# Optimization experiments

Measured on AMD Instinct MI355X. Metric: run time of the kernel, lower is better.

The kernel has to match this reference:

```python
import jax, jax.numpy as jnp
import numpy as np

N_HEADS = 8
N_POINTS = 4


def _bilinear_sample(vl, g, Hl, Wl):
    # vl: [B, nH, Hl*Wl, hd] level values; g: [B, Q, nH, P, 2] sampling locs in [0,1] (x, y)
    # Emulates torch grid_sample(mode='bilinear', padding_mode='zeros', align_corners=False)
    B, Q, nH, P, _ = g.shape
    hd = vl.shape[-1]
    x = g[..., 0] * Wl - 0.5
    y = g[..., 1] * Hl - 0.5
    x0f = jnp.floor(x)
    y0f = jnp.floor(y)
    x0 = x0f.astype(jnp.int32)
    y0 = y0f.astype(jnp.int32)
    wx1 = x - x0f
    wy1 = y - y0f

    def corner(xi, yi, w):
        valid = (xi >= 0) & (xi < Wl) & (yi >= 0) & (yi < Hl)
        idx = jnp.clip(yi, 0, Hl - 1) * Wl + jnp.clip(xi, 0, Wl - 1)  # [B,Q,nH,P]
        idx = idx.transpose(0, 2, 1, 3).reshape(B, nH, Q * P)
        gathered = jnp.take_along_axis(vl, idx[..., None], axis=2)  # [B,nH,Q*P,hd]
        wm = (w * valid.astype(w.dtype)).transpose(0, 2, 1, 3).reshape(B, nH, Q * P)
        return gathered * wm[..., None]

    s = (corner(x0, y0, (1.0 - wx1) * (1.0 - wy1))
         + corner(x0 + 1, y0, wx1 * (1.0 - wy1))
         + corner(x0, y0 + 1, (1.0 - wx1) * wy1)
         + corner(x0 + 1, y0 + 1, wx1 * wy1))
    return s.reshape(B, nH, Q, P, hd)


def setup_inputs() -> dict:
    key = jax.random.key(0)
    ks = jax.random.split(key, 12)
    B, Q, D = 32, 300, 256
    L, P, nH = 4, N_POINTS, N_HEADS
    shapes = np.array([[80, 80], [40, 40], [20, 20], [10, 10]], dtype=np.int32)
    V = int((shapes[:, 0] * shapes[:, 1]).sum())  # 8500
    lsi = np.concatenate([[0], np.cumsum(shapes[:, 0] * shapes[:, 1])[:-1]]).astype(np.int32)
    sd = 1.0 / np.sqrt(D)
    return {
        'query': jax.random.normal(ks[0], (B, Q, D), jnp.float32),
        'reference_points': jax.random.uniform(ks[1], (B, Q, L, 2), jnp.float32),
        'value': jax.random.normal(ks[2], (B, V, D), jnp.float32),
        'spatial_shapes': jnp.asarray(shapes),
        'level_start_index': jnp.asarray(lsi),
        'W_off': jax.random.normal(ks[3], (D, nH * L * P * 2), jnp.float32) * sd,
        'b_off': jax.random.normal(ks[4], (nH * L * P * 2,), jnp.float32) * 0.5,
        'W_attn': jax.random.normal(ks[5], (D, nH * L * P), jnp.float32) * sd,
        'b_attn': jax.random.normal(ks[6], (nH * L * P,), jnp.float32) * 0.1,
        'W_val': jax.random.normal(ks[7], (D, D), jnp.float32) * sd,
        'b_val': jnp.zeros((D,), jnp.float32),
        'W_out': jax.random.normal(ks[8], (D, D), jnp.float32) * sd,
        'b_out': jnp.zeros((D,), jnp.float32),
    }


def reference(query, reference_points, value, spatial_shapes, level_start_index,
              W_off, b_off, W_attn, b_attn, W_val, b_val, W_out, b_out):
    shapes = np.asarray(spatial_shapes)  # static level shapes
    B, Q, D = query.shape
    nH, P = N_HEADS, N_POINTS
    L = shapes.shape[0]
    hd = D // nH

    val = value @ W_val + b_val  # [B,V,D]
    val = val.reshape(B, -1, nH, hd).transpose(0, 2, 1, 3)  # [B,nH,V,hd]

    off = (query @ W_off + b_off).reshape(B, Q, nH, L, P, 2)
    attn = jax.nn.softmax((query @ W_attn + b_attn).reshape(B, Q, nH, L * P), axis=-1)
    attn = attn.reshape(B, Q, nH, L, P)

    # normalizer is (W_l, H_l)
    norm = jnp.asarray(np.stack([shapes[:, 1], shapes[:, 0]], -1), jnp.float32)  # [L,2]
    loc = reference_points[:, :, None, :, None, :] + off / norm[None, None, None, :, None, :]

    out = jnp.zeros((B, Q, nH, hd), query.dtype)
    start = 0
    for lvl in range(L):
        Hl, Wl = int(shapes[lvl, 0]), int(shapes[lvl, 1])
        vl = val[:, :, start:start + Hl * Wl, :]  # [B,nH,HW,hd]
        sampled = _bilinear_sample(vl, loc[:, :, :, lvl], Hl, Wl)  # [B,nH,Q,P,hd]
        out = out + jnp.einsum('bnqpd,bqnp->bqnd', sampled, attn[:, :, :, lvl])
        start += Hl * Wl

    return out.reshape(B, Q, D) @ W_out + b_out
```

## Files before the change

### kernel.cpp

```cpp
#include <hip/hip_runtime.h>
#include <math.h>
#include <stdint.h>

#define NB 32
#define NQ 300
#define ND 256
#define NH 8
#define HD 32
#define NL 4
#define NP 4
#define V_TOT 8500
#define BQ_TOT (NB*NQ)
#define MVAL (NB*V_TOT)
#define NOA 384

typedef short v8s __attribute__((ext_vector_type(8)));
typedef float v4f __attribute__((ext_vector_type(4)));

#define AS1 __attribute__((address_space(1)))
#define AS3 __attribute__((address_space(3)))

__device__ __forceinline__ void copy16_async(const void* g, void* l) {
#if __has_builtin(__builtin_amdgcn_global_load_lds)
    __builtin_amdgcn_global_load_lds((const AS1 unsigned int*)g,
                                     (AS3 unsigned int*)l, 16, 0, 0);
#else
    *(uint4*)l = *(const uint4*)g;
#endif
}

__device__ __forceinline__ unsigned short f2bf_rne(float x) {
    unsigned u = __float_as_uint(x);
    u += 0x7fffu + ((u >> 16) & 1u);
    return (unsigned short)(u >> 16);
}
__device__ __forceinline__ float bf2f(unsigned short b) {
    return __uint_as_float(((unsigned)b) << 16);
}

__device__ __forceinline__ int swz_pos(int n, int k) {
    const int base = k & ~31;
    const int o = (k >> 3) & 3;
    const int op = o ^ ((n >> 1) & 3);
    return n * 256 + base + (op << 3) + (k & 7);
}

__global__ __launch_bounds__(256) void prep_weights(
    const float* __restrict__ W_val, const float* __restrict__ W_off,
    const float* __restrict__ W_attn, const float* __restrict__ W_out,
    const float* __restrict__ b_off, const float* __restrict__ b_attn,
    unsigned short* __restrict__ Bval_h, unsigned short* __restrict__ Bval_l,
    unsigned short* __restrict__ Boa_h,  unsigned short* __restrict__ Boa_l,
    unsigned short* __restrict__ Bout_h, unsigned short* __restrict__ Bout_l,
    float* __restrict__ b_oa)
{
    const int t = blockIdx.x * 256 + threadIdx.x;
    if (t < 65536) {
        const int n = t >> 8, k = t & 255;
        const float x = W_val[k * 256 + n];
        const unsigned short hi = f2bf_rne(x);
        const unsigned short lo = f2bf_rne(x - bf2f(hi));
        const int p = swz_pos(n, k);
        Bval_h[p] = hi; Bval_l[p] = lo;
    } else if (t < 65536 + 98304) {
        const int t2 = t - 65536;
        const int n = t2 >> 8, k = t2 & 255;
        const float x = (n < 256) ? W_off[k * 256 + n] : W_attn[k * 128 + (n - 256)];
        const unsigned short hi = f2bf_rne(x);
        const unsigned short lo = f2bf_rne(x - bf2f(hi));
        const int p = swz_pos(n, k);
        Boa_h[p] = hi; Boa_l[p] = lo;
    } else if (t < 229376) {
        const int t3 = t - 163840;
        const int n = t3 >> 8, k = t3 & 255;
        const float x = W_out[k * 256 + n];
        const unsigned short hi = f2bf_rne(x);
        const unsigned short lo = f2bf_rne(x - bf2f(hi));
        const int p = swz_pos(n, k);
        Bout_h[p] = hi; Bout_l[p] = lo;
    } else {
        const int t4 = t - 229376;
        if (t4 < NOA) b_oa[t4] = (t4 < 256) ? b_off[t4] : b_attn[t4 - 256];
    }
}

__global__ __launch_bounds__(256) void gemm_a32(
    const float* __restrict__ A,
    const unsigned short* __restrict__ Bh,
    const unsigned short* __restrict__ Bl,
    const float* __restrict__ bias,
    float* __restrict__ Cf,
    unsigned short* __restrict__ Cb,
    int ldc, int mode)
{
    __shared__ unsigned short Ah[2][128][40];
    __shared__ unsigned short Al[2][128][40];
    __shared__ unsigned short Bs[2][2][128][32];

    const int tid  = threadIdx.x;
    const int row0 = blockIdx.x * 128;
    const int col0 = blockIdx.y * 128;
    const int wave = tid >> 6;
    const int lane = tid & 63;
    const int wm   = (wave >> 1) * 64;
    const int wn   = (wave & 1) * 64;
    const int m16  = lane & 15;
    const int quad = lane >> 4;

    int rr[2], oo[2];
#pragma unroll
    for (int i = 0; i < 2; ++i) {
        const int idx = tid + i * 256;
        rr[i] = idx >> 2;
        oo[i] = (idx & 3) << 3;
    }

    v4f acc[4][4] = {};
    float fe[2][8];

#pragma unroll
    for (int c = 0; c < 2; ++c) {
        const int linear = (wave * 2 + c) * 1024 + lane * 16;
        const int n   = linear >> 6;
        const int off = linear & 63;
        copy16_async((const char*)Bh + ((size_t)(col0 + n) * 256 + 0) * 2 + off,
                     (char*)&Bs[0][0][0][0] + linear);
        copy16_async((const char*)Bl + ((size_t)(col0 + n) * 256 + 0) * 2 + off,
                     (char*)&Bs[0][1][0][0] + linear);
    }
#pragma unroll
    for (int i = 0; i < 2; ++i) {
        const float4 f0 = *(const float4*)(A + (size_t)(row0 + rr[i]) * 256 + oo[i]);
        const float4 f1 = *(const float4*)(A + (size_t)(row0 + rr[i]) * 256 + oo[i] + 4);
        fe[i][0] = f0.x; fe[i][1] = f0.y; fe[i][2] = f0.z; fe[i][3] = f0.w;
        fe[i][4] = f1.x; fe[i][5] = f1.y; fe[i][6] = f1.z; fe[i][7] = f1.w;
    }
#pragma unroll
    for (int i = 0; i < 2; ++i) {
        unsigned hpk[4], lpk[4];
#pragma unroll
        for (int e = 0; e < 4; ++e) {
            const unsigned u0 = __float_as_uint(fe[i][2*e]);
            const unsigned u1 = __float_as_uint(fe[i][2*e+1]);
            hpk[e] = (u0 >> 16) | (u1 & 0xffff0000u);
            const float l0 = fe[i][2*e]   - __uint_as_float(u0 & 0xffff0000u);
            const float l1 = fe[i][2*e+1] - __uint_as_float(u1 & 0xffff0000u);
            lpk[e] = (__float_as_uint(l0) >> 16) | (__float_as_uint(l1) & 0xffff0000u);
        }
        *(uint4*)&Ah[0][rr[i]][oo[i]] = make_uint4(hpk[0], hpk[1], hpk[2], hpk[3]);
        *(uint4*)&Al[0][rr[i]][oo[i]] = make_uint4(lpk[0], lpk[1], lpk[2], lpk[3]);
    }

    __syncthreads();

    for (int t = 0; t < 8; ++t) {
        const int buf = t & 1;
        const int nb  = buf ^ 1;
        const int k1  = (t + 1) << 5;

        if (t < 7) {
#pragma unroll
            for (int i = 0; i < 2; ++i) {
                const float4 f0 = *(const float4*)(A + (size_t)(row0 + rr[i]) * 256 + k1 + oo[i]);
                const float4 f1 = *(const float4*)(A + (size_t)(row0 + rr[i]) * 256 + k1 + oo[i] + 4);
                fe[i][0] = f0.x; fe[i][1] = f0.y; fe[i][2] = f0.z; fe[i][3] = f0.w;
                fe[i][4] = f1.x; fe[i][5] = f1.y; fe[i][6] = f1.z; fe[i][7] = f1.w;
            }
#pragma unroll
            for (int c = 0; c < 2; ++c) {
                const int linear = (wave * 2 + c) * 1024 + lane * 16;
                const int n   = linear >> 6;
                const int off = linear & 63;
                copy16_async((const char*)Bh + ((size_t)(col0 + n) * 256 + k1) * 2 + off,
                             (char*)&Bs[nb][0][0][0] + linear);
                copy16_async((const char*)Bl + ((size_t)(col0 + n) * 256 + k1) * 2 + off,
                             (char*)&Bs[nb][1][0][0] + linear);
            }
        }

        v8s ah[4], al[4], bh[4], bl[4];
#pragma unroll
        for (int i = 0; i < 4; ++i) {
            ah[i] = *(v8s*)&Ah[buf][wm + i * 16 + m16][quad * 8];
            al[i] = *(v8s*)&Al[buf][wm + i * 16 + m16][quad * 8];
            const int n  = wn + i * 16 + m16;
            const int ko = (quad ^ ((n >> 1) & 3)) << 3;
            bh[i] = *(v8s*)&Bs[buf][0][n][ko];
            bl[i] = *(v8s*)&Bs[buf][1][n][ko];
        }

#pragma unroll
        for (int i = 0; i < 4; ++i)
#pragma unroll
            for (int j = 0; j < 4; ++j) {
                acc[i][j] = __builtin_amdgcn_mfma_f32_16x16x32_bf16(ah[i], bh[j], acc[i][j], 0, 0, 0);
                acc[i][j] = __builtin_amdgcn_mfma_f32_16x16x32_bf16(ah[i], bl[j], acc[i][j], 0, 0, 0);
                acc[i][j] = __builtin_amdgcn_mfma_f32_16x16x32_bf16(al[i], bh[j], acc[i][j], 0, 0, 0);
            }

        if (t < 7) {
#pragma unroll
            for (int i = 0; i < 2; ++i) {
                unsigned hpk[4], lpk[4];
#pragma unroll
                for (int e = 0; e < 4; ++e) {
                    const unsigned u0 = __float_as_uint(fe[i][2*e]);
                    const unsigned u1 = __float_as_uint(fe[i][2*e+1]);
                    hpk[e] = (u0 >> 16) | (u1 & 0xffff0000u);
                    const float l0 = fe[i][2*e]   - __uint_as_float(u0 & 0xffff0000u);
                    const float l1 = fe[i][2*e+1] - __uint_as_float(u1 & 0xffff0000u);
                    lpk[e] = (__float_as_uint(l0) >> 16) | (__float_as_uint(l1) & 0xffff0000u);
                }
                *(uint4*)&Ah[nb][rr[i]][oo[i]] = make_uint4(hpk[0], hpk[1], hpk[2], hpk[3]);
                *(uint4*)&Al[nb][rr[i]][oo[i]] = make_uint4(lpk[0], lpk[1], lpk[2], lpk[3]);
            }
        }

        __syncthreads();
    }

#pragma unroll
    for (int j = 0; j < 4; ++j) {
        const int cl = col0 + wn + j * 16 + m16;
        const float bb = bias[cl];
        if (mode == 0) {
#pragma unroll
            for (int i = 0; i < 4; ++i)
#pragma unroll
                for (int r = 0; r < 4; ++r) {
                    const int R = row0 + wm + i * 16 + quad * 4 + r;
                    Cf[(size_t)R * ldc + cl] = acc[i][j][r] + bb;
                }
        } else {
            const int h  = cl >> 5;
            const int dh = cl & 31;
#pragma unroll
            for (int i = 0; i < 4; ++i)
#pragma unroll
                for (int r = 0; r < 4; ++r) {
                    const int R = row0 + wm + i * 16 + quad * 4 + r;
                    const unsigned b = (unsigned)R / V_TOT;
                    const int v = R - (int)b * V_TOT;
                    Cb[(((size_t)(b * NH + h)) * V_TOT + v) * HD + dh] =
                        f2bf_rne(acc[i][j][r] + bb);
                }
        }
    }
}

__global__ __launch_bounds__(256) void gemm_a16(
    const unsigned short* __restrict__ A,
    const unsigned short* __restrict__ Bh,
    const unsigned short* __restrict__ Bl,
    const float* __restrict__ bias,
    float* __restrict__ C, int ldc)
{
    __shared__ unsigned short As[2][128][32];
    __shared__ unsigned short Bs[2][2][128][32];

    const int tid  = threadIdx.x;
    const int row0 = blockIdx.x * 128;
    const int col0 = blockIdx.y * 128;
    const int wave = tid >> 6;
    const int lane = tid & 63;
    const int wm   = (wave >> 1) * 64;
    const int wn   = (wave & 1) * 64;
    const int m16  = lane & 15;
    const int quad = lane >> 4;

    v4f acc[4][4] = {};

#pragma unroll
    for (int c = 0; c < 2; ++c) {
        const int linear = (wave * 2 + c) * 1024 + lane * 16;
        const int n   = linear >> 6;
        const int off = linear & 63;
        copy16_async((const char*)A  + ((size_t)(row0 + n) * 256 + 0) * 2 + off,
                     (char*)&As[0][0][0] + linear);
        copy16_async((const char*)Bh + ((size_t)(col0 + n) * 256 + 0) * 2 + off,
                     (char*)&Bs[0][0][0][0] + linear);
        copy16_async((const char*)Bl + ((size_t)(col0 + n) * 256 + 0) * 2 + off,
                     (char*)&Bs[0][1][0][0] + linear);
    }
    __syncthreads();

    for (int t = 0; t < 8; ++t) {
        const int buf = t & 1;
        const int nb  = buf ^ 1;
        const int k1  = (t + 1) << 5;

        if (t < 7) {
#pragma unroll
            for (int c = 0; c < 2; ++c) {
                const int linear = (wave * 2 + c) * 1024 + lane * 16;
                const int n   = linear >> 6;
                const int off = linear & 63;
                copy16_async((const char*)A  + ((size_t)(row0 + n) * 256 + k1) * 2 + off,
                             (char*)&As[nb][0][0] + linear);
                copy16_async((const char*)Bh + ((size_t)(col0 + n) * 256 + k1) * 2 + off,
                             (char*)&Bs[nb][0][0][0] + linear);
                copy16_async((const char*)Bl + ((size_t)(col0 + n) * 256 + k1) * 2 + off,
                             (char*)&Bs[nb][1][0][0] + linear);
            }
        }

        v8s a[4], bh[4], bl[4];
#pragma unroll
        for (int i = 0; i < 4; ++i) {
            const int r  = wm + i * 16 + m16;
            const int ka = (quad ^ ((r >> 1) & 3)) << 3;
            a[i] = *(v8s*)&As[buf][r][ka];
            const int n  = wn + i * 16 + m16;
            const int kb = (quad ^ ((n >> 1) & 3)) << 3;
            bh[i] = *(v8s*)&Bs[buf][0][n][kb];
            bl[i] = *(v8s*)&Bs[buf][1][n][kb];
        }
#pragma unroll
        for (int i = 0; i < 4; ++i)
#pragma unroll
            for (int j = 0; j < 4; ++j) {
                acc[i][j] = __builtin_amdgcn_mfma_f32_16x16x32_bf16(a[i], bh[j], acc[i][j], 0, 0, 0);
                acc[i][j] = __builtin_amdgcn_mfma_f32_16x16x32_bf16(a[i], bl[j], acc[i][j], 0, 0, 0);
            }

        __syncthreads();
    }

#pragma unroll
    for (int j = 0; j < 4; ++j) {
        const int cl = col0 + wn + j * 16 + m16;
        const float bb = bias[cl];
#pragma unroll
        for (int i = 0; i < 4; ++i)
#pragma unroll
            for (int r = 0; r < 4; ++r) {
                const int R = row0 + wm + i * 16 + quad * 4 + r;
                C[(size_t)R * ldc + cl] = acc[i][j][r] + bb;
            }
    }
}

__global__ __launch_bounds__(256) void sample_kernel(
    const float* __restrict__ refp,
    const float* __restrict__ offattn,
    const unsigned short* __restrict__ val,
    unsigned short* __restrict__ pre)
{
    const int t  = blockIdx.x * 256 + threadIdx.x;
    const int d8 = t & 3;
    const int h  = (t >> 2) & 7;
    const int bq = t >> 5;
    const int b  = bq / NQ;

    const float* rp = refp + (size_t)bq * 8;
    const float* op = offattn + (size_t)bq * 384 + h * 32;
    const float* ap = offattn + (size_t)bq * 384 + 256 + h * 16;

    float aw[16];
    float m = -1e30f;
#pragma unroll
    for (int i = 0; i < 16; ++i) { aw[i] = ap[i]; m = fmaxf(m, aw[i]); }
    float s = 0.f;
#pragma unroll
    for (int i = 0; i < 16; ++i) { aw[i] = __expf(aw[i] - m); s += aw[i]; }
    const float inv = 1.f / s;
#pragma unroll
    for (int i = 0; i < 16; ++i) aw[i] *= inv;

    const int Hs[4] = {80, 40, 20, 10};
    const int St[4] = {0, 6400, 8000, 8400};

    float acc[8] = {};
#pragma unroll
    for (int l = 0; l < NL; ++l) {
        const int Wl = Hs[l], Hl = Hs[l];
        const float fW = (float)Wl, fH = (float)Hl;
        const float rx = rp[l * 2 + 0];
        const float ry = rp[l * 2 + 1];
        const unsigned short* vb =
            val + (((size_t)(b * NH + h)) * V_TOT + St[l]) * HD + d8 * 8;
#pragma unroll
        for (int p = 0; p < NP; ++p) {
            const float ox = op[l * 8 + p * 2 + 0];
            const float oy = op[l * 8 + p * 2 + 1];
            const float w  = aw[l * 4 + p];
            const float x = fmaf(rx, fW, ox) - 0.5f;
            const float y = fmaf(ry, fH, oy) - 0.5f;
            const float x0f = floorf(x), y0f = floorf(y);
            const int   x0 = (int)x0f,  y0 = (int)y0f;
            const float wx1 = x - x0f,  wy1 = y - y0f;
            const float wx0 = 1.f - wx1, wy0 = 1.f - wy1;
#pragma unroll
            for (int cy = 0; cy < 2; ++cy) {
#pragma unroll
                for (int cx = 0; cx < 2; ++cx) {
                    const int xi = x0 + cx;
                    const int yi = y0 + cy;
                    float cw = (cx ? wx1 : wx0) * (cy ? wy1 : wy0) * w;
                    const bool valid = (xi >= 0) && (xi < Wl) && (yi >= 0) && (yi < Hl);
                    cw = valid ? cw : 0.f;
                    const int xc = xi < 0 ? 0 : (xi > Wl - 1 ? Wl - 1 : xi);
                    const int yc = yi < 0 ? 0 : (yi > Hl - 1 ? Hl - 1 : yi);
                    const uint4 g = *(const uint4*)(vb + (size_t)(yc * Wl + xc) * HD);
                    const unsigned gu[4] = {g.x, g.y, g.z, g.w};
#pragma unroll
                    for (int e = 0; e < 4; ++e) {
                        acc[2*e]   = fmaf(cw, __uint_as_float(gu[e] << 16),        acc[2*e]);
                        acc[2*e+1] = fmaf(cw, __uint_as_float(gu[e] & 0xffff0000u), acc[2*e+1]);
                    }
                }
            }
        }
    }

    unsigned o[4];
#pragma unroll
    for (int e = 0; e < 4; ++e)
        o[e] = (unsigned)f2bf_rne(acc[2*e]) | ((unsigned)f2bf_rne(acc[2*e+1]) << 16);
    const int octswz = d8 ^ ((bq >> 1) & 3);
    *(uint4*)(pre + (size_t)bq * 256 + h * 32 + octswz * 8) =
        make_uint4(o[0], o[1], o[2], o[3]);
}

extern "C" void kernel_launch(void* const* d_in, const int* in_sizes, int n_in,
                              void* d_out, int out_size, void* d_ws, size_t ws_size,
                              hipStream_t stream)
{
    const float* query  = (const float*)d_in[0];
    const float* refp   = (const float*)d_in[1];
    const float* value  = (const float*)d_in[2];
    const float* W_off  = (const float*)d_in[5];
    const float* b_off  = (const float*)d_in[6];
    const float* W_attn = (const float*)d_in[7];
    const float* b_attn = (const float*)d_in[8];
    const float* W_val  = (const float*)d_in[9];
    const float* b_val  = (const float*)d_in[10];
    const float* W_out  = (const float*)d_in[11];
    const float* b_out  = (const float*)d_in[12];
    float* out = (float*)d_out;

    char* ws = (char*)d_ws;
    unsigned short* val     = (unsigned short*)ws;
    float*          offattn = (float*)(ws + 139264000);
    unsigned short* pre     = (unsigned short*)(ws + 154009600);
    unsigned short* Bval_h  = (unsigned short*)(ws + 158924800);
    unsigned short* Bval_l  = Bval_h + 65536;
    unsigned short* Boa_h   = Bval_l + 65536;
    unsigned short* Boa_l   = Boa_h + 98304;
    unsigned short* Bout_h  = Boa_l + 98304;
    unsigned short* Bout_l  = Bout_h + 65536;
    float*          b_oa    = (float*)(Bout_l + 65536);

    const dim3 blk(256);

    prep_weights<<<dim3(898), blk, 0, stream>>>(
        W_val, W_off, W_attn, W_out, b_off, b_attn,
        Bval_h, Bval_l, Boa_h, Boa_l, Bout_h, Bout_l, b_oa);

    gemm_a32<<<dim3(MVAL / 128, 2), blk, 0, stream>>>(
        value, Bval_h, Bval_l, b_val, nullptr, val, 0, 1);

    gemm_a32<<<dim3(BQ_TOT / 128, 3), blk, 0, stream>>>(
        query, Boa_h, Boa_l, b_oa, offattn, nullptr, NOA, 0);

    sample_kernel<<<dim3((BQ_TOT * 32) / 256), blk, 0, stream>>>(
        refp, offattn, val, pre);

    gemm_a16<<<dim3(BQ_TOT / 128, 2), blk, 0, stream>>>(
        pre, Bout_h, Bout_l, b_out, out, 256);
}
```

Baseline: 629.0 us.

## Load GEMM A operand directly into MFMA registers, dropping LDS staging

The fp32 A tile is no longer converted and staged through shared memory. Each lane now loads its own MFMA fragment straight from global memory and splits it into bf16 hi/lo in registers. This removes the LDS writes and reads for A and shrinks shared memory use, and launch bounds now ask for 3 blocks per SM to raise occupancy. In exchange, rows are loaded redundantly across the two column waves, each lane reads 32-byte strided segments, and the global loads for A are no longer prefetched one step ahead, so their latency is exposed.

```diff
diff --git a/kernel.cpp b/kernel.cpp
--- a/kernel.cpp
+++ b/kernel.cpp
@@ -36,6 +36,12 @@
 }
 __device__ __forceinline__ float bf2f(unsigned short b) {
     return __uint_as_float(((unsigned)b) << 16);
+}
+
+__device__ __forceinline__ v8s pack4(unsigned a, unsigned b, unsigned c, unsigned d) {
+    union { unsigned u[4]; v8s s; } t;
+    t.u[0] = a; t.u[1] = b; t.u[2] = c; t.u[3] = d;
+    return t.s;
 }
 
 __device__ __forceinline__ int swz_pos(int n, int k) {
@@ -84,7 +90,7 @@
     }
 }
 
-__global__ __launch_bounds__(256) void gemm_a32(
+__global__ __launch_bounds__(256, 3) void gemm_a32(
     const float* __restrict__ A,
     const unsigned short* __restrict__ Bh,
     const unsigned short* __restrict__ Bl,
@@ -93,8 +99,6 @@
     unsigned short* __restrict__ Cb,
     int ldc, int mode)
 {
-    __shared__ unsigned short Ah[2][128][40];
-    __shared__ unsigned short Al[2][128][40];
     __shared__ unsigned short Bs[2][2][128][32];
 
     const int tid  = threadIdx.x;
@@ -107,16 +111,9 @@
     const int m16  = lane & 15;
     const int quad = lane >> 4;
 
-    int rr[2], oo[2];
-#pragma unroll
-    for (int i = 0; i < 2; ++i) {
-        const int idx = tid + i * 256;
-        rr[i] = idx >> 2;
-        oo[i] = (idx & 3) << 3;
-    }
+    const float* Abase = A + (size_t)(row0 + wm + m16) * 256 + quad * 8;
 
     v4f acc[4][4] = {};
-    float fe[2][8];
 
 #pragma unroll
     for (int c = 0; c < 2; ++c) {
@@ -128,61 +125,36 @@
         copy16_async((const char*)Bl + ((size_t)(col0 + n) * 256 + 0) * 2 + off,
                      (char*)&Bs[0][1][0][0] + linear);
     }
-#pragma unroll
-    for (int i = 0; i < 2; ++i) {
-        const float4 f0 = *(const float4*)(A + (size_t)(row0 + rr[i]) * 256 + oo[i]);
-        const float4 f1 = *(const float4*)(A + (size_t)(row0 + rr[i]) * 256 + oo[i] + 4);
-        fe[i][0] = f0.x; fe[i][1] = f0.y; fe[i][2] = f0.z; fe[i][3] = f0.w;
-        fe[i][4] = f1.x; fe[i][5] = f1.y; fe[i][6] = f1.z; fe[i][7] = f1.w;
-    }
-#pragma unroll
-    for (int i = 0; i < 2; ++i) {
-        unsigned hpk[4], lpk[4];
-#pragma unroll
-        for (int e = 0; e < 4; ++e) {
-            const unsigned u0 = __float_as_uint(fe[i][2*e]);
-            const unsigned u1 = __float_as_uint(fe[i][2*e+1]);
-            hpk[e] = (u0 >> 16) | (u1 & 0xffff0000u);
-            const float l0 = fe[i][2*e]   - __uint_as_float(u0 & 0xffff0000u);
-            const float l1 = fe[i][2*e+1] - __uint_as_float(u1 & 0xffff0000u);
-            lpk[e] = (__float_as_uint(l0) >> 16) | (__float_as_uint(l1) & 0xffff0000u);
-        }
-        *(uint4*)&Ah[0][rr[i]][oo[i]] = make_uint4(hpk[0], hpk[1], hpk[2], hpk[3]);
-        *(uint4*)&Al[0][rr[i]][oo[i]] = make_uint4(lpk[0], lpk[1], lpk[2], lpk[3]);
-    }
-
     __syncthreads();
 
     for (int t = 0; t < 8; ++t) {
         const int buf = t & 1;
-        const int nb  = buf ^ 1;
-        const int k1  = (t + 1) << 5;
+        const int k0  = t << 5;
 
         if (t < 7) {
-#pragma unroll
-            for (int i = 0; i < 2; ++i) {
-                const float4 f0 = *(const float4*)(A + (size_t)(row0 + rr[i]) * 256 + k1 + oo[i]);
-                const float4 f1 = *(const float4*)(A + (size_t)(row0 + rr[i]) * 256 + k1 + oo[i] + 4);
-                fe[i][0] = f0.x; fe[i][1] = f0.y; fe[i][2] = f0.z; fe[i][3] = f0.w;
-                fe[i][4] = f1.x; fe[i][5] = f1.y; fe[i][6] = f1.z; fe[i][7] = f1.w;
-            }
 #pragma unroll
             for (int c = 0; c < 2; ++c) {
                 const int linear = (wave * 2 + c) * 1024 + lane * 16;
                 const int n   = linear >> 6;
                 const int off = linear & 63;
-                copy16_async((const char*)Bh + ((size_t)(col0 + n) * 256 + k1) * 2 + off,
-                             (char*)&Bs[nb][0][0][0] + linear);
-                copy16_async((const char*)Bl + ((size_t)(col0 + n) * 256 + k1) * 2 + off,
-                             (char*)&Bs[nb][1][0][0] + linear);
-            }
-        }
-
-        v8s ah[4], al[4], bh[4], bl[4];
+                copy16_async((const char*)Bh + ((size_t)(col0 + n) * 256 + k0 + 32) * 2 + off,
+                             (char*)&Bs[buf ^ 1][0][0][0] + linear);
+                copy16_async((const char*)Bl + ((size_t)(col0 + n) * 256 + k0 + 32) * 2 + off,
+                             (char*)&Bs[buf ^ 1][1][0][0] + linear);
+            }
+        }
+
+        float4 f0[4], f1[4];
 #pragma unroll
         for (int i = 0; i < 4; ++i) {
-            ah[i] = *(v8s*)&Ah[buf][wm + i * 16 + m16][quad * 8];
-            al[i] = *(v8s*)&Al[buf][wm + i * 16 + m16][quad * 8];
+            const float* ap = Abase + ((size_t)i * 16) * 256 + k0;
+            f0[i] = *(const float4*)ap;
+            f1[i] = *(const float4*)(ap + 4);
+        }
+
+        v8s bh[4], bl[4];
+#pragma unroll
+        for (int i = 0; i < 4; ++i) {
             const int n  = wn + i * 16 + m16;
             const int ko = (quad ^ ((n >> 1) & 3)) << 3;
             bh[i] = *(v8s*)&Bs[buf][0][n][ko];
@@ -190,29 +162,26 @@
         }
 
 #pragma unroll
-        for (int i = 0; i < 4; ++i)
+        for (int i = 0; i < 4; ++i) {
+            const float fe[8] = {f0[i].x, f0[i].y, f0[i].z, f0[i].w,
+                                 f1[i].x, f1[i].y, f1[i].z, f1[i].w};
+            unsigned hpk[4], lpk[4];
+#pragma unroll
+            for (int e = 0; e < 4; ++e) {
+                const unsigned u0 = __float_as_uint(fe[2*e]);
+                const unsigned u1 = __float_as_uint(fe[2*e+1]);
+                hpk[e] = (u0 >> 16) | (u1 & 0xffff0000u);
+                const float l0 = fe[2*e]   - __uint_as_float(u0 & 0xffff0000u);
+                const float l1 = fe[2*e+1] - __uint_as_float(u1 & 0xffff0000u);
+                lpk[e] = (__float_as_uint(l0) >> 16) | (__float_as_uint(l1) & 0xffff0000u);
+            }
+            const v8s ah = pack4(hpk[0], hpk[1], hpk[2], hpk[3]);
+            const v8s al = pack4(lpk[0], lpk[1], lpk[2], lpk[3]);
 #pragma unroll
             for (int j = 0; j < 4; ++j) {
-                acc[i][j] = __builtin_amdgcn_mfma_f32_16x16x32_bf16(ah[i], bh[j], acc[i][j], 0, 0, 0);
-                acc[i][j] = __builtin_amdgcn_mfma_f32_16x16x32_bf16(ah[i], bl[j], acc[i][j], 0, 0, 0);
-                acc[i][j] = __builtin_amdgcn_mfma_f32_16x16x32_bf16(al[i], bh[j], acc[i][j], 0, 0, 0);
-            }
-
-        if (t < 7) {
-#pragma unroll
-            for (int i = 0; i < 2; ++i) {
-                unsigned hpk[4], lpk[4];
-#pragma unroll
-                for (int e = 0; e < 4; ++e) {
-                    const unsigned u0 = __float_as_uint(fe[i][2*e]);
-                    const unsigned u1 = __float_as_uint(fe[i][2*e+1]);
-                    hpk[e] = (u0 >> 16) | (u1 & 0xffff0000u);
-                    const float l0 = fe[i][2*e]   - __uint_as_float(u0 & 0xffff0000u);
-                    const float l1 = fe[i][2*e+1] - __uint_as_float(u1 & 0xffff0000u);
-                    lpk[e] = (__float_as_uint(l0) >> 16) | (__float_as_uint(l1) & 0xffff0000u);
-                }
-                *(uint4*)&Ah[nb][rr[i]][oo[i]] = make_uint4(hpk[0], hpk[1], hpk[2], hpk[3]);
-                *(uint4*)&Al[nb][rr[i]][oo[i]] = make_uint4(lpk[0], lpk[1], lpk[2], lpk[3]);
+                acc[i][j] = __builtin_amdgcn_mfma_f32_16x16x32_bf16(ah, bh[j], acc[i][j], 0, 0, 0);
+                acc[i][j] = __builtin_amdgcn_mfma_f32_16x16x32_bf16(ah, bl[j], acc[i][j], 0, 0, 0);
+                acc[i][j] = __builtin_amdgcn_mfma_f32_16x16x32_bf16(al, bh[j], acc[i][j], 0, 0, 0);
             }
         }
 
```

After: 676.6 us. 1.08x slower.
